# Performance work log

Measured on AMD Instinct MI355X. Metric: run time of the kernel, lower is better.

## Reference

```python
import jax, jax.numpy as jnp
import numpy as np

B, SEQ, PRED, DM = 16, 2048, 2048, 64
P = SEQ + PRED            # PointNum = 4096, per-node feature length
NLAYER, HID = 3, 4096     # MLPNums, ggdmodel hidden sizes
NH, HS = 16, 4096         # NumAttentionHeads, HiddenSize
G_CONST, K = 1.0, 8
NN = DM * DM              # 4096 == P, MHSA input dim (required by original code)


def setup_inputs() -> dict:
    key = jax.random.key(0)
    ks = jax.random.split(key, 11)
    s_mlp = 1.0 / np.sqrt(P).astype(np.float32)
    s_att = 1.0 / np.sqrt(NN).astype(np.float32)
    s_out = 1.0 / np.sqrt(HS).astype(np.float32)
    return {
        "x": jax.random.normal(ks[0], (B, P, DM), jnp.float32),
        "W_mlp": jax.random.normal(ks[1], (NLAYER, P, HID), jnp.float32) * s_mlp,
        "b_mlp": jnp.zeros((NLAYER, HID), jnp.float32),
        "Wq": jax.random.normal(ks[2], (NN, HS), jnp.float32) * s_att,
        "bq": jnp.zeros((HS,), jnp.float32),
        "Wk": jax.random.normal(ks[3], (NN, HS), jnp.float32) * s_att,
        "bk": jnp.zeros((HS,), jnp.float32),
        "Wv": jax.random.normal(ks[4], (NN, HS), jnp.float32) * s_att,
        "bv": jnp.zeros((HS,), jnp.float32),
        "Wo": jax.random.normal(ks[5], (HS, HS), jnp.float32) * s_out,
        "bo": jnp.zeros((HS,), jnp.float32),
    }


def _grav_adj(h):
    # h: [B, N, D] node features -> symmetrized, top-K masked gravity adjacency [B, N, N]
    norm = jnp.linalg.norm(h, axis=-1)                      # [B, N]
    m = jnp.sum(h, axis=-1) / norm                          # node "mass"
    sim = jnp.einsum('bnd,bmd->bnm', h, h) / (norm[:, :, None] * norm[:, None, :])
    F = G_CONST * m[:, :, None] * m[:, None, :] * sim * sim  # gravity matrix
    kth = jax.lax.top_k(F, K)[0][..., -1:]                  # per-row Kth largest value
    F = jnp.where(F >= kth, F, 0.0)                         # keep only top-K per row
    F = jnp.maximum(F, 0.0)                                 # ReLU
    return 0.5 * (F + jnp.swapaxes(F, -1, -2))              # symmetrize


def reference(x, W_mlp, b_mlp, Wq, bq, Wk, bk, Wv, bv, Wo, bo):
    h = jnp.swapaxes(x, 1, 2)                               # [B, N=DM, P]
    adjs = [_grav_adj(h)]
    for l in range(NLAYER):                                 # each MLP applied to the same h
        hv = h @ W_mlp[l] + b_mlp[l]                        # [B, N, HID]
        adjs.append(_grav_adj(hv))
    A = jnp.stack(adjs, axis=1)                             # [B, L, N, N], L = NLAYER + 1
    Lseq = A.shape[1]
    tok = A.reshape(B, Lseq, NN)                            # L tokens of dim N*N
    dh = HS // NH
    q = (tok @ Wq + bq).reshape(B, Lseq, NH, dh)
    k = (tok @ Wk + bk).reshape(B, Lseq, NH, dh)
    v = (tok @ Wv + bv).reshape(B, Lseq, NH, dh)
    scores = jnp.einsum('blhd,bmhd->bhlm', q, k) / np.sqrt(dh).astype(np.float32)
    attn = jax.nn.softmax(scores, axis=-1)
    ctx = jnp.einsum('bhlm,bmhd->blhd', attn, v).reshape(B, Lseq, HS)
    out = ctx @ Wo + bo                                     # [B, L, HS]
    return jnp.where(out > 0.5, out, 0.0)
```

## Files before the change

kernel.cpp:

```cpp
#include <hip/hip_runtime.h>
#include <math.h>


#define B16 16
#define PDIM 4096
#define NNODE 64
#define NCHUNK 32
#define KCG 128

typedef __attribute__((ext_vector_type(8))) short bf16x8;
typedef __attribute__((ext_vector_type(4))) float f32x4;
typedef __attribute__((ext_vector_type(4))) unsigned short us4;
typedef __attribute__((ext_vector_type(8))) unsigned short us8;

__device__ inline void split2(float x, unsigned short& h, unsigned short& l) {
  unsigned u = __float_as_uint(x);
  unsigned hu = (u + 0x7fffu + ((u >> 16) & 1u)) & 0xffff0000u;
  h = (unsigned short)(hu >> 16);
  float lo = x - __uint_as_float(hu);
  unsigned u2 = __float_as_uint(lo);
  l = (unsigned short)((u2 + 0x7fffu + ((u2 >> 16) & 1u)) >> 16);
}

__device__ inline void gload16(const void* g, void* lds) {
  __builtin_amdgcn_global_load_lds((const unsigned int*)g, (unsigned int*)lds, 16, 0, 0);
}

__global__ __launch_bounds__(256) void k_transpose(const float* __restrict__ x,
                                                   float* __restrict__ h,
                                                   unsigned short* __restrict__ AhT,
                                                   unsigned short* __restrict__ AlT,
                                                   int mode) {
  __shared__ float t[64][65];
  int b = blockIdx.y;
  int p0 = blockIdx.x * 64;
  const float* xb = x + (size_t)b * PDIM * NNODE;
#pragma unroll
  for (int i = 0; i < 16; ++i) {
    int e = i * 256 + threadIdx.x;
    int p = e >> 6, n = e & 63;
    t[p][n] = xb[(size_t)p0 * 64 + e];
  }
  __syncthreads();
  if (mode != 2) {
    float* hb = h + (size_t)b * NNODE * PDIM;
#pragma unroll
    for (int i = 0; i < 16; ++i) {
      int e = i * 256 + threadIdx.x;
      int n = e >> 6, p = e & 63;
      hb[(size_t)n * PDIM + p0 + p] = t[p][n];
    }
  }
  if (mode == 0) return;
#pragma unroll
  for (int j = 0; j < 2; ++j) {
    int cid = j * 256 + threadIdx.x;
    int n2 = cid >> 3, kg8 = cid & 7;
    us8 hv_, lv_;
#pragma unroll
    for (int e = 0; e < 8; ++e) {
      unsigned short hh, ll;
      split2(t[kg8 * 8 + e][n2], hh, ll);
      hv_[e] = hh; lv_[e] = ll;
    }
    int m = b * 64 + n2;
    int ks = (p0 >> 5) + (kg8 >> 2);
    size_t idx = (((size_t)(m >> 7) * 128 + ks) * 8 + ((m >> 4) & 7)) * 512 +
                 (size_t)((n2 & 15) + 16 * (kg8 & 3)) * 8;
    *(us8*)&AhT[idx] = hv_;
    *(us8*)&AlT[idx] = lv_;
  }
}

__global__ __launch_bounds__(256) void k_wsplit(const float* __restrict__ W,
                                                unsigned short* __restrict__ WhT,
                                                unsigned short* __restrict__ WlT) {
  __shared__ float Wt[32][132];
  int nb = blockIdx.x, kb = blockIdx.y;
  int tid = threadIdx.x;
#pragma unroll
  for (int i = 0; i < 4; ++i) {
    int idx = i * 256 + tid;
    int row = idx >> 5, c4 = idx & 31;
    float4 v = *(const float4*)&W[(size_t)(kb * 32 + row) * 4096 + nb * 128 + c4 * 4];
    *(float4*)&Wt[row][c4 * 4] = v;
  }
  __syncthreads();
#pragma unroll
  for (int j = 0; j < 2; ++j) {
    int cid = j * 256 + tid;
    int nl = cid & 127, kg = cid >> 7;
    us8 hv_, lv_;
#pragma unroll
    for (int e = 0; e < 8; ++e) {
      unsigned short hh, ll;
      split2(Wt[kg * 8 + e][nl], hh, ll);
      hv_[e] = hh; lv_[e] = ll;
    }
    size_t idx = (((size_t)nb * 128 + kb) * 8 + (nl >> 4)) * 512 +
                 (size_t)((nl & 15) + 16 * kg) * 8;
    *(us8*)&WhT[idx] = hv_;
    *(us8*)&WlT[idx] = lv_;
  }
}

__global__ __launch_bounds__(512, 4) void k_gemm_bf16(
    const unsigned short* __restrict__ Ah, const unsigned short* __restrict__ Al,
    const unsigned short* __restrict__ Bh, const unsigned short* __restrict__ Bl,
    float* __restrict__ Cp, int Ksteps, int ksplit, int N, int mstore) {
  __shared__ unsigned short sAh[2][4096], sAl[2][4096];
  __shared__ unsigned short sBh[2][4096], sBl[2][4096];
  int tid = threadIdx.x;
  int l = tid & 63, wid = tid >> 6;
  int wr = wid >> 2, wc = wid & 3;
  int nb = blockIdx.x, mb = blockIdx.y, z = blockIdx.z;
  int spp = Ksteps / ksplit;
  int ks0 = z * spp;

  const size_t abase = ((size_t)mb * Ksteps + ks0) * 4096 + tid * 8;
  const size_t bbase = ((size_t)nb * Ksteps + ks0) * 4096 + tid * 8;

  f32x4 acc[4][2];
#pragma unroll
  for (int i = 0; i < 4; ++i)
#pragma unroll
    for (int j = 0; j < 2; ++j) acc[i][j] = (f32x4){0.f, 0.f, 0.f, 0.f};

  gload16(Ah + abase, &sAh[0][tid * 8]);
  gload16(Al + abase, &sAl[0][tid * 8]);
  gload16(Bh + bbase, &sBh[0][tid * 8]);
  gload16(Bl + bbase, &sBl[0][tid * 8]);
  __syncthreads();

  int buf = 0;
  for (int t = 0; t < spp; ++t) {
    if (t + 1 < spp) {
      size_t off = (size_t)(t + 1) * 4096;
      gload16(Ah + abase + off, &sAh[buf ^ 1][tid * 8]);
      gload16(Al + abase + off, &sAl[buf ^ 1][tid * 8]);
      gload16(Bh + bbase + off, &sBh[buf ^ 1][tid * 8]);
      gload16(Bl + bbase + off, &sBl[buf ^ 1][tid * 8]);
    }
    bf16x8 ah[4], al4[4], bh2[2], bl2[2];
#pragma unroll
    for (int mt = 0; mt < 4; ++mt) {
      ah[mt]  = *(const bf16x8*)&sAh[buf][(wr * 4 + mt) * 512 + l * 8];
      al4[mt] = *(const bf16x8*)&sAl[buf][(wr * 4 + mt) * 512 + l * 8];
    }
#pragma unroll
    for (int nt = 0; nt < 2; ++nt) {
      bh2[nt] = *(const bf16x8*)&sBh[buf][(wc * 2 + nt) * 512 + l * 8];
      bl2[nt] = *(const bf16x8*)&sBl[buf][(wc * 2 + nt) * 512 + l * 8];
    }
#pragma unroll
    for (int mt = 0; mt < 4; ++mt)
#pragma unroll
      for (int nt = 0; nt < 2; ++nt) {
        acc[mt][nt] = __builtin_amdgcn_mfma_f32_16x16x32_bf16(ah[mt],  bh2[nt], acc[mt][nt], 0, 0, 0);
        acc[mt][nt] = __builtin_amdgcn_mfma_f32_16x16x32_bf16(ah[mt],  bl2[nt], acc[mt][nt], 0, 0, 0);
        acc[mt][nt] = __builtin_amdgcn_mfma_f32_16x16x32_bf16(al4[mt], bh2[nt], acc[mt][nt], 0, 0, 0);
      }
    __syncthreads();
    buf ^= 1;
  }

  int n0 = nb * 128, m0 = mb * 128;
  float* Cz = Cp + (size_t)z * mstore * N;
#pragma unroll
  for (int mt = 0; mt < 4; ++mt)
#pragma unroll
    for (int nt = 0; nt < 2; ++nt) {
      int col = n0 + wc * 32 + nt * 16 + (l & 15);
#pragma unroll
      for (int r = 0; r < 4; ++r) {
        int row = m0 + wr * 64 + mt * 16 + ((l >> 4) << 2) + r;
        if (row < mstore) Cz[(size_t)row * N + col] = acc[mt][nt][r];
      }
    }
}

__global__ __launch_bounds__(512) void k_gemm_wsf32(
    const unsigned short* __restrict__ Ah, const unsigned short* __restrict__ Al,
    const float* __restrict__ W0, const float* __restrict__ W1,
    const float* __restrict__ W2, float* __restrict__ Cp, int ksplit) {
  __shared__ unsigned short sAh[2][2048], sAl[2][2048];
  __shared__ unsigned short sBh[2][4096], sBl[2][4096];
  int tid = threadIdx.x;
  int l = tid & 63, wid = tid >> 6;
  int wr = wid >> 2, wc = wid & 3;
  int nb = blockIdx.x, z = blockIdx.z;
  int mat = z / ksplit, kz = z - mat * ksplit;
  const float* W = (mat == 0) ? W0 : ((mat == 1) ? W1 : W2);
  int nsteps = 128 / ksplit;
  int ks0 = kz * nsteps;
  int n0 = nb * 128;

  const float* wbase = W + (size_t)((l >> 4) * 8) * 4096 + n0 + wid * 16 + (l & 15);
  int sidx = wid * 512 + l * 8;

  f32x4 acc[2][2];
#pragma unroll
  for (int i = 0; i < 2; ++i)
#pragma unroll
    for (int j = 0; j < 2; ++j) acc[i][j] = (f32x4){0.f, 0.f, 0.f, 0.f};

  {
    if (tid < 256) gload16(Ah + (size_t)ks0 * 4096 + tid * 8, &sAh[0][tid * 8]);
    else           gload16(Al + (size_t)ks0 * 4096 + (tid - 256) * 8, &sAl[0][(tid - 256) * 8]);
    float wv[8];
#pragma unroll
    for (int e = 0; e < 8; ++e) wv[e] = wbase[(size_t)ks0 * 131072 + (size_t)e * 4096];
    us8 hi, lo;
#pragma unroll
    for (int e = 0; e < 8; ++e) {
      unsigned short hh, ll;
      split2(wv[e], hh, ll);
      hi[e] = hh; lo[e] = ll;
    }
    *(us8*)&sBh[0][sidx] = hi;
    *(us8*)&sBl[0][sidx] = lo;
  }
  __syncthreads();

  int buf = 0;
  for (int t = 0; t < nsteps; ++t) {
    bool more = (t + 1 < nsteps);
    float wv[8];
    if (more) {
      int ks = ks0 + t + 1;
      if (tid < 256) gload16(Ah + (size_t)ks * 4096 + tid * 8, &sAh[buf ^ 1][tid * 8]);
      else           gload16(Al + (size_t)ks * 4096 + (tid - 256) * 8, &sAl[buf ^ 1][(tid - 256) * 8]);
#pragma unroll
      for (int e = 0; e < 8; ++e) wv[e] = wbase[(size_t)ks * 131072 + (size_t)e * 4096];
    }
    bf16x8 aH[2], aL[2], bH[2], bL[2];
#pragma unroll
    for (int i = 0; i < 2; ++i) {
      aH[i] = *(const bf16x8*)&sAh[buf][(wr * 2 + i) * 512 + l * 8];
      aL[i] = *(const bf16x8*)&sAl[buf][(wr * 2 + i) * 512 + l * 8];
      bH[i] = *(const bf16x8*)&sBh[buf][(wc * 2 + i) * 512 + l * 8];
      bL[i] = *(const bf16x8*)&sBl[buf][(wc * 2 + i) * 512 + l * 8];
    }
#pragma unroll
    for (int i = 0; i < 2; ++i)
#pragma unroll
      for (int j = 0; j < 2; ++j) {
        acc[i][j] = __builtin_amdgcn_mfma_f32_16x16x32_bf16(aH[i], bH[j], acc[i][j], 0, 0, 0);
        acc[i][j] = __builtin_amdgcn_mfma_f32_16x16x32_bf16(aH[i], bL[j], acc[i][j], 0, 0, 0);
        acc[i][j] = __builtin_amdgcn_mfma_f32_16x16x32_bf16(aL[i], bH[j], acc[i][j], 0, 0, 0);
      }
    if (more) {
      us8 hi, lo;
#pragma unroll
      for (int e = 0; e < 8; ++e) {
        unsigned short hh, ll;
        split2(wv[e], hh, ll);
        hi[e] = hh; lo[e] = ll;
      }
      *(us8*)&sBh[buf ^ 1][sidx] = hi;
      *(us8*)&sBl[buf ^ 1][sidx] = lo;
    }
    __syncthreads();
    buf ^= 1;
  }

  float* Cz = Cp + (size_t)z * 262144;
#pragma unroll
  for (int i = 0; i < 2; ++i)
#pragma unroll
    for (int j = 0; j < 2; ++j) {
      int col = n0 + wc * 32 + j * 16 + (l & 15);
#pragma unroll
      for (int r = 0; r < 4; ++r) {
        int row = (wr * 2 + i) * 16 + ((l >> 4) << 2) + r;
        Cz[(size_t)row * 4096 + col] = acc[i][j][r];
      }
    }
}

__global__ __launch_bounds__(256) void k_red_mlp_split(const float* __restrict__ Cp,
                                                       const float* __restrict__ bias,
                                                       unsigned short* __restrict__ hvh,
                                                       unsigned short* __restrict__ hvl) {
  int c = blockIdx.x * 256 + threadIdx.x;
  int m = c >> 9, kc = c & 511;
  int k0 = kc * 8;
  const float* p = Cp + (size_t)m * 4096 + k0;
  us8 hv_, lv_;
#pragma unroll
  for (int e = 0; e < 8; ++e) {
    float v = p[e] + p[e + 4194304] + bias[k0 + e];
    unsigned short hh, ll;
    split2(v, hh, ll);
    hv_[e] = hh; lv_[e] = ll;
  }
  int batch = m >> 6, rr = m & 63;
  size_t idx = (size_t)batch * 262144 + (size_t)(kc >> 2) * 2048 +
               (size_t)(rr >> 4) * 512 + (size_t)((rr & 15) + 16 * (kc & 3)) * 8;
  *(us8*)&hvh[idx] = hv_;
  *(us8*)&hvl[idx] = lv_;
}

__global__ __launch_bounds__(256) void k_gram_mfma(
    const unsigned short* __restrict__ Zh, const unsigned short* __restrict__ Zl,
    float* __restrict__ Gp, float* __restrict__ Sp,
    int bs1, int ks_stride, int nsteps) {
  __shared__ unsigned short sZh[2][2048], sZl[2][2048];
  int z = blockIdx.x, b = blockIdx.y;
  int tid = threadIdx.x;
  int l = tid & 63, w = tid >> 6;
  size_t zbase = (size_t)(b >> 1) * 524288 + (size_t)(b & 1) * bs1;
  int ks0 = z * nsteps;

  f32x4 acc[4], racc;
#pragma unroll
  for (int j = 0; j < 4; ++j) acc[j] = (f32x4){0.f, 0.f, 0.f, 0.f};
  racc = (f32x4){0.f, 0.f, 0.f, 0.f};
  bf16x8 ones;
#pragma unroll
  for (int e = 0; e < 8; ++e) ones[e] = (short)0x3F80;

  gload16(Zh + zbase + (size_t)ks0 * ks_stride + tid * 8, &sZh[0][tid * 8]);
  gload16(Zl + zbase + (size_t)ks0 * ks_stride + tid * 8, &sZl[0][tid * 8]);
  __syncthreads();

  int buf = 0;
  for (int t = 0; t < nsteps; ++t) {
    if (t + 1 < nsteps) {
      size_t off = zbase + (size_t)(ks0 + t + 1) * ks_stride + tid * 8;
      gload16(Zh + off, &sZh[buf ^ 1][tid * 8]);
      gload16(Zl + off, &sZl[buf ^ 1][tid * 8]);
    }
    bf16x8 bh[4], bl4[4];
#pragma unroll
    for (int nt = 0; nt < 4; ++nt) {
      bh[nt]  = *(const bf16x8*)&sZh[buf][nt * 512 + l * 8];
      bl4[nt] = *(const bf16x8*)&sZl[buf][nt * 512 + l * 8];
    }
    bf16x8 ah = bh[w], al = bl4[w];
#pragma unroll
    for (int nt = 0; nt < 4; ++nt) {
      acc[nt] = __builtin_amdgcn_mfma_f32_16x16x32_bf16(ah, bh[nt], acc[nt], 0, 0, 0);
      acc[nt] = __builtin_amdgcn_mfma_f32_16x16x32_bf16(ah, bl4[nt], acc[nt], 0, 0, 0);
      acc[nt] = __builtin_amdgcn_mfma_f32_16x16x32_bf16(al, bh[nt], acc[nt], 0, 0, 0);
    }
    racc = __builtin_amdgcn_mfma_f32_16x16x32_bf16(ah, ones, racc, 0, 0, 0);
    racc = __builtin_amdgcn_mfma_f32_16x16x32_bf16(al, ones, racc, 0, 0, 0);
    __syncthreads();
    buf ^= 1;
  }

  float* Gz = Gp + ((size_t)z * B16 + b) * 4096;
#pragma unroll
  for (int nt = 0; nt < 4; ++nt) {
    int col = nt * 16 + (l & 15);
#pragma unroll
    for (int r = 0; r < 4; ++r) {
      int row = w * 16 + ((l >> 4) << 2) + r;
      Gz[row * 64 + col] = acc[nt][r];
    }
  }
  if ((l & 15) == 0) {
    float* Sz = Sp + ((size_t)z * B16 + b) * 64;
#pragma unroll
    for (int r = 0; r < 4; ++r) Sz[w * 16 + ((l >> 4) << 2) + r] = racc[r];
  }
}

__global__ __launch_bounds__(256) void k_gred8(const float* __restrict__ Gp,
                                               const float* __restrict__ Sp,
                                               float* __restrict__ G,
                                               float* __restrict__ S, int slot) {
  int idx = blockIdx.x * 256 + threadIdx.x;
  if (idx < 65536) {
    float s = 0.f;
#pragma unroll
    for (int c = 0; c < 8; ++c) s += Gp[(size_t)c * 65536 + idx];
    G[(size_t)slot * 65536 + idx] = s;
  } else if (idx < 66560) {
    int i2 = idx - 65536;
    float s = 0.f;
#pragma unroll
    for (int c = 0; c < 8; ++c) s += Sp[(size_t)c * 1024 + i2];
    S[(size_t)slot * 1024 + i2] = s;
  }
}

__global__ __launch_bounds__(256) void k_redN(const float* __restrict__ Cp,
                                              const float* __restrict__ bias,
                                              float* __restrict__ dst,
                                              int nparts, int thr) {
  int idx = blockIdx.x * 256 + threadIdx.x;
  float s = bias[idx & 4095];
  for (int p = 0; p < nparts; ++p) s += Cp[(size_t)p * 262144 + idx];
  if (thr) s = (s > 0.5f) ? s : 0.f;
  dst[idx] = s;
}

__device__ inline float wmax64(float v) {
#pragma unroll
  for (int off = 32; off; off >>= 1) v = fmaxf(v, __shfl_xor(v, off));
  return v;
}

__global__ __launch_bounds__(256) void k_adj_t(const float* __restrict__ G,
                                               const float* __restrict__ S,
                                               unsigned short* __restrict__ tokh,
                                               unsigned short* __restrict__ tokl) {
  __shared__ float Fm[64][64];
  __shared__ float nrm[64], mm[64];
  int b = blockIdx.x >> 2, lz = blockIdx.x & 3;
  int tid = threadIdx.x;
  int j = tid & 63, w = tid >> 6;
  const float* Gb = G + ((size_t)lz * B16 + b) * 4096;
  const float* Sb = S + ((size_t)lz * B16 + b) * 64;
  if (tid < 64) {
    float nj = sqrtf(Gb[tid * 64 + tid]);
    nrm[tid] = nj;
    mm[tid] = Sb[tid] / nj;
  }
  __syncthreads();
  for (int i = w; i < 64; i += 4) {
    float g = Gb[i * 64 + j];
    float sim = g / (nrm[i] * nrm[j]);
    Fm[i][j] = mm[i] * mm[j] * sim * sim;
  }
  __syncthreads();
  for (int i = w; i < 64; i += 4) {
    float f = Fm[i][j];
    int cnt = 0;
#pragma unroll
    for (int u4 = 0; u4 < 16; ++u4) {
      float4 q = *(const float4*)&Fm[i][u4 * 4];
      cnt += (q.x > f) + (q.y > f) + (q.z > f) + (q.w > f);
    }
    float cand = (cnt <= 7) ? f : INFINITY;
#pragma unroll
    for (int off = 32; off; off >>= 1) cand = fminf(cand, __shfl_xor(cand, off));
    float fm = (f >= cand) ? fmaxf(f, 0.f) : 0.f;
    Fm[i][j] = fm;
  }
  __syncthreads();
  int r = b * 4 + lz;
  int mt = r >> 4, rl = r & 15;
#pragma unroll
  for (int c = 0; c < 2; ++c) {
    int cid = tid * 2 + c;
    int jj0 = cid >> 3, g = cid & 7;
    us8 hv_, lv_;
#pragma unroll
    for (int e = 0; e < 8; ++e) {
      int kcol = g * 8 + e;
      float val = 0.5f * (Fm[jj0][kcol] + Fm[kcol][jj0]);
      unsigned short hh, ll;
      split2(val, hh, ll);
      hv_[e] = hh; lv_[e] = ll;
    }
    int ks = jj0 * 2 + (g >> 2);
    size_t idx = ((size_t)ks * 8 + mt) * 512 + (size_t)(rl + 16 * (g & 3)) * 8;
    *(us8*)&tokh[idx] = hv_;
    *(us8*)&tokl[idx] = lv_;
  }
}

__global__ __launch_bounds__(64) void k_attn_t(const float* __restrict__ q,
                                               const float* __restrict__ k,
                                               const float* __restrict__ v,
                                               unsigned short* __restrict__ ctxh,
                                               unsigned short* __restrict__ ctxl) {
  __shared__ float cb[4][256];
  int hd = blockIdx.x, b = blockIdx.y;
  int t = threadIdx.x;
  float qr[4][4], kr[4][4], vr[4][4];
#pragma unroll
  for (int l = 0; l < 4; ++l)
#pragma unroll
    for (int s = 0; s < 4; ++s) {
      size_t off = ((size_t)(b * 4 + l)) * 4096 + hd * 256 + t + s * 64;
      qr[l][s] = q[off]; kr[l][s] = k[off]; vr[l][s] = v[off];
    }
  float sc[4][4];
#pragma unroll
  for (int l = 0; l < 4; ++l)
#pragma unroll
    for (int m = 0; m < 4; ++m) {
      float p = 0.f;
#pragma unroll
      for (int s = 0; s < 4; ++s) p = fmaf(qr[l][s], kr[m][s], p);
#pragma unroll
      for (int off = 32; off; off >>= 1) p += __shfl_xor(p, off);
      sc[l][m] = p * (1.0f / 16.0f);
    }
  float at[4][4];
#pragma unroll
  for (int l = 0; l < 4; ++l) {
    float mx = fmaxf(fmaxf(sc[l][0], sc[l][1]), fmaxf(sc[l][2], sc[l][3]));
    float e0 = expf(sc[l][0] - mx), e1 = expf(sc[l][1] - mx);
    float e2 = expf(sc[l][2] - mx), e3 = expf(sc[l][3] - mx);
    float d = e0 + e1 + e2 + e3;
    at[l][0] = e0 / d; at[l][1] = e1 / d; at[l][2] = e2 / d; at[l][3] = e3 / d;
  }
#pragma unroll
  for (int l = 0; l < 4; ++l)
#pragma unroll
    for (int s = 0; s < 4; ++s) {
      float c = 0.f;
#pragma unroll
      for (int m = 0; m < 4; ++m) c = fmaf(at[l][m], vr[m][s], c);
      cb[l][s * 64 + t] = c;
    }
  __syncthreads();
  int lq = t >> 4, c16 = t & 15;
  int mt = b >> 2, rl = (b & 3) * 4 + lq;
#pragma unroll
  for (int e8 = 0; e8 < 2; ++e8) {
    us8 hv_, lv_;
#pragma unroll
    for (int e = 0; e < 8; ++e) {
      unsigned short hh, ll;
      split2(cb[lq][c16 * 16 + e8 * 8 + e], hh, ll);
      hv_[e] = hh; lv_[e] = ll;
    }
    int ks = hd * 8 + (c16 >> 1);
    size_t idx = ((size_t)ks * 8 + mt) * 512 + (size_t)(rl + 16 * ((c16 * 2 + e8) & 3)) * 8;
    *(us8*)&ctxh[idx] = hv_;
    *(us8*)&ctxl[idx] = lv_;
  }
}

__global__ __launch_bounds__(256) void k_gram_partial(const float* __restrict__ Z,
                                                      float* __restrict__ Gp,
                                                      float* __restrict__ Sp) {
  __shared__ float Zt[KCG][68];
  int c = blockIdx.x, b = blockIdx.y;
  int tid = threadIdx.x;
  const float* Zb = Z + (size_t)b * NNODE * PDIM + c * KCG;
#pragma unroll
  for (int i = 0; i < 32; ++i) {
    int e = i * 256 + tid;
    int r = e >> 7, kk = e & 127;
    Zt[kk][r] = Zb[(size_t)r * PDIM + kk];
  }
  __syncthreads();
  int ii = tid >> 2, j0 = (tid & 3) << 4;
  float acc[16] = {};
  for (int kk = 0; kk < KCG; ++kk) {
    float zi = Zt[kk][ii];
    float4 z0 = *(const float4*)&Zt[kk][j0 + 0];
    float4 z1 = *(const float4*)&Zt[kk][j0 + 4];
    float4 z2 = *(const float4*)&Zt[kk][j0 + 8];
    float4 z3 = *(const float4*)&Zt[kk][j0 + 12];
    acc[0] = fmaf(zi, z0.x, acc[0]);   acc[1] = fmaf(zi, z0.y, acc[1]);
    acc[2] = fmaf(zi, z0.z, acc[2]);   acc[3] = fmaf(zi, z0.w, acc[3]);
    acc[4] = fmaf(zi, z1.x, acc[4]);   acc[5] = fmaf(zi, z1.y, acc[5]);
    acc[6] = fmaf(zi, z1.z, acc[6]);   acc[7] = fmaf(zi, z1.w, acc[7]);
    acc[8] = fmaf(zi, z2.x, acc[8]);   acc[9] = fmaf(zi, z2.y, acc[9]);
    acc[10] = fmaf(zi, z2.z, acc[10]); acc[11] = fmaf(zi, z2.w, acc[11]);
    acc[12] = fmaf(zi, z3.x, acc[12]); acc[13] = fmaf(zi, z3.y, acc[13]);
    acc[14] = fmaf(zi, z3.z, acc[14]); acc[15] = fmaf(zi, z3.w, acc[15]);
  }
  float* gp = Gp + ((size_t)c * B16 + b) * 4096 + ii * 64 + j0;
#pragma unroll
  for (int j = 0; j < 16; ++j) gp[j] = acc[j];
  if (tid < 64) {
    float s = 0.f;
    for (int kk = 0; kk < KCG; ++kk) s += Zt[kk][tid];
    Sp[((size_t)c * B16 + b) * 64 + tid] = s;
  }
}

__global__ __launch_bounds__(256) void k_gram_reduce(const float* __restrict__ Gp,
                                                     const float* __restrict__ Sp,
                                                     float* __restrict__ G,
                                                     float* __restrict__ S, int slot) {
  int idx = blockIdx.x * 256 + threadIdx.x;
  if (idx < B16 * 4096) {
    float s = 0.f;
    for (int c = 0; c < NCHUNK; ++c) s += Gp[(size_t)c * (B16 * 4096) + idx];
    G[(size_t)slot * (B16 * 4096) + idx] = s;
  } else {
    int idx2 = idx - B16 * 4096;
    float s = 0.f;
    for (int c = 0; c < NCHUNK; ++c) s += Sp[(size_t)c * (B16 * 64) + idx2];
    S[(size_t)slot * (B16 * 64) + idx2] = s;
  }
}

__global__ __launch_bounds__(256) void k_gemm_mfma(
    const float* __restrict__ A, const float* __restrict__ B0,
    const float* __restrict__ B1, const float* __restrict__ B2,
    const float* __restrict__ bias, float* __restrict__ C,
    int mrows, int mstore, int N, int K, int ksplit) {
  __shared__ __align__(16) unsigned short sA[2][8][64][8];
  __shared__ __align__(16) unsigned short sB[2][8][64][8];
  int z = blockIdx.z;
  int mat = z / ksplit, ks = z - mat * ksplit;
  const float* Bm = (mat == 0) ? B0 : ((mat == 1) ? B1 : B2);
  int kchunk = K / ksplit;
  int k0 = ks * kchunk, k1 = k0 + kchunk;
  int tid = threadIdx.x;
  int l = tid & 63;
  int wr = (tid >> 7) & 1, wc = (tid >> 6) & 1;
  int m0 = blockIdx.y * 128, n0g = blockIdx.x * 128;
  bool activeM = (m0 + wr * 64) < mstore;
  int am = tid >> 1;
  int arow = m0 + am; if (arow >= mrows) arow = mrows - 1;
  const float* Arow = A + (size_t)arow * K;
  int amt = am >> 4;
  int bk = tid >> 3;
  int bnb = (tid & 7) * 4;
  int bg = bk >> 3, bslot = bk & 7;
  f32x4 acc[4][4];
#pragma unroll
  for (int i = 0; i < 4; ++i)
#pragma unroll
    for (int j = 0; j < 4; ++j) acc[i][j] = (f32x4){0.f, 0.f, 0.f, 0.f};
  for (int kb = k0; kb < k1; kb += 32) {
    __syncthreads();
#pragma unroll
    for (int i = 0; i < 4; ++i) {
      int kq = (tid & 1) * 4 + i * 8;
      float4 a = *(const float4*)(Arow + kb + kq);
      unsigned short h0, h1, h2, h3, l0, l1, l2, l3;
      split2(a.x, h0, l0); split2(a.y, h1, l1);
      split2(a.z, h2, l2); split2(a.w, h3, l3);
      int lane_t = (am & 15) + 16 * (kq >> 3);
      int sb = kq & 4;
      *(us4*)&sA[0][amt][lane_t][sb] = (us4){h0, h1, h2, h3};
      *(us4*)&sA[1][amt][lane_t][sb] = (us4){l0, l1, l2, l3};
    }
    {
      const float* Brow = Bm + (size_t)(kb + bk) * N + n0g;
#pragma unroll
      for (int i = 0; i < 4; ++i) {
        int n = bnb + i * 32;
        int nt = n >> 4, nr = n & 15;
        float4 b = *(const float4*)(Brow + n);
        float be[4] = {b.x, b.y, b.z, b.w};
#pragma unroll
        for (int e = 0; e < 4; ++e) {
          unsigned short hh, ll;
          split2(be[e], hh, ll);
          sB[0][nt][nr + e + 16 * bg][bslot] = hh;
          sB[1][nt][nr + e + 16 * bg][bslot] = ll;
        }
      }
    }
    __syncthreads();
    if (!activeM) continue;
    bf16x8 ah[4], al[4], bh[4], bl[4];
#pragma unroll
    for (int t = 0; t < 4; ++t) {
      ah[t] = *(const bf16x8*)&sA[0][wr * 4 + t][l][0];
      al[t] = *(const bf16x8*)&sA[1][wr * 4 + t][l][0];
      bh[t] = *(const bf16x8*)&sB[0][wc * 4 + t][l][0];
      bl[t] = *(const bf16x8*)&sB[1][wc * 4 + t][l][0];
    }
#pragma unroll
    for (int mt = 0; mt < 4; ++mt)
#pragma unroll
      for (int nt = 0; nt < 4; ++nt) {
        acc[mt][nt] = __builtin_amdgcn_mfma_f32_16x16x32_bf16(ah[mt], bh[nt], acc[mt][nt], 0, 0, 0);
        acc[mt][nt] = __builtin_amdgcn_mfma_f32_16x16x32_bf16(ah[mt], bl[nt], acc[mt][nt], 0, 0, 0);
        acc[mt][nt] = __builtin_amdgcn_mfma_f32_16x16x32_bf16(al[mt], bh[nt], acc[mt][nt], 0, 0, 0);
      }
  }
  if (!activeM) return;
  float* Cz = C + (size_t)z * mstore * N;
#pragma unroll
  for (int mt = 0; mt < 4; ++mt)
#pragma unroll
    for (int nt = 0; nt < 4; ++nt) {
      int col = n0g + wc * 64 + nt * 16 + (l & 15);
      float badd = bias ? bias[col] : 0.f;
#pragma unroll
      for (int r = 0; r < 4; ++r) {
        int row = m0 + wr * 64 + mt * 16 + ((l >> 4) << 2) + r;
        if (row < mstore) Cz[(size_t)row * N + col] = acc[mt][nt][r] + badd;
      }
    }
}

__global__ __launch_bounds__(64) void k_adj_fb(const float* __restrict__ G,
                                               const float* __restrict__ S,
                                               float* __restrict__ tok) {
  __shared__ float Fm[64][64];
  __shared__ float nrm[64], mm[64];
  int b = blockIdx.x >> 2, lz = blockIdx.x & 3;
  int j = threadIdx.x;
  const float* Gb = G + ((size_t)lz * B16 + b) * 4096;
  const float* Sb = S + ((size_t)lz * B16 + b) * 64;
  float nj = sqrtf(Gb[j * 64 + j]);
  nrm[j] = nj;
  mm[j] = Sb[j] / nj;
  __syncthreads();
  for (int i = 0; i < 64; ++i) {
    float g = Gb[i * 64 + j];
    float sim = g / (nrm[i] * nj);
    float F = mm[i] * mm[j] * sim * sim;
    float v = F;
    bool act = true;
    float kth = 0.f;
#pragma unroll
    for (int it = 0; it < 8; ++it) {
      float mv = wmax64(act ? v : -INFINITY);
      kth = mv;
      unsigned long long ball = __ballot(act && (v == mv));
      int first = __ffsll(ball) - 1;
      if (j == first) act = false;
    }
    float fm = (F >= kth) ? F : 0.f;
    Fm[i][j] = fmaxf(fm, 0.f);
  }
  __syncthreads();
  float* tb = tok + ((size_t)b * 4 + lz) * 4096;
  for (int i = 0; i < 64; ++i) tb[i * 64 + j] = 0.5f * (Fm[i][j] + Fm[j][i]);
}

__global__ __launch_bounds__(256) void k_qkv_reduce(const float* __restrict__ Cp,
                                                    const float* __restrict__ bq,
                                                    const float* __restrict__ bk,
                                                    const float* __restrict__ bv,
                                                    float* __restrict__ q,
                                                    float* __restrict__ k,
                                                    float* __restrict__ v) {
  int idx = blockIdx.x * 256 + threadIdx.x;
  int mat = idx >> 18;
  int rn = idx & ((1 << 18) - 1);
  int n = rn & 4095;
  const float* base = Cp + (size_t)mat * 4 * 262144;
  float s = base[rn] + base[rn + 262144] + base[rn + 2 * 262144] + base[rn + 3 * 262144];
  if (mat == 0) q[rn] = s + bq[n];
  else if (mat == 1) k[rn] = s + bk[n];
  else v[rn] = s + bv[n];
}

__global__ __launch_bounds__(64) void k_attn_fb(const float* __restrict__ q,
                                                const float* __restrict__ k,
                                                const float* __restrict__ v,
                                                float* __restrict__ ctx) {
  int hd = blockIdx.x, b = blockIdx.y;
  int t = threadIdx.x;
  float qr[4][4], kr[4][4], vr[4][4];
#pragma unroll
  for (int l = 0; l < 4; ++l)
#pragma unroll
    for (int s = 0; s < 4; ++s) {
      size_t off = ((size_t)(b * 4 + l)) * 4096 + hd * 256 + t + s * 64;
      qr[l][s] = q[off]; kr[l][s] = k[off]; vr[l][s] = v[off];
    }
  float sc[4][4];
#pragma unroll
  for (int l = 0; l < 4; ++l)
#pragma unroll
    for (int m = 0; m < 4; ++m) {
      float p = 0.f;
#pragma unroll
      for (int s = 0; s < 4; ++s) p = fmaf(qr[l][s], kr[m][s], p);
#pragma unroll
      for (int off = 32; off; off >>= 1) p += __shfl_xor(p, off);
      sc[l][m] = p * (1.0f / 16.0f);
    }
  float at[4][4];
#pragma unroll
  for (int l = 0; l < 4; ++l) {
    float mx = fmaxf(fmaxf(sc[l][0], sc[l][1]), fmaxf(sc[l][2], sc[l][3]));
    float e0 = expf(sc[l][0] - mx), e1 = expf(sc[l][1] - mx);
    float e2 = expf(sc[l][2] - mx), e3 = expf(sc[l][3] - mx);
    float d = e0 + e1 + e2 + e3;
    at[l][0] = e0 / d; at[l][1] = e1 / d; at[l][2] = e2 / d; at[l][3] = e3 / d;
  }
#pragma unroll
  for (int l = 0; l < 4; ++l)
#pragma unroll
    for (int s = 0; s < 4; ++s) {
      float c = 0.f;
#pragma unroll
      for (int m = 0; m < 4; ++m) c = fmaf(at[l][m], vr[m][s], c);
      ctx[((size_t)(b * 4 + l)) * 4096 + hd * 256 + t + s * 64] = c;
    }
}

__global__ __launch_bounds__(256) void k_out_reduce(const float* __restrict__ Cp,
                                                    const float* __restrict__ bo,
                                                    float* __restrict__ out) {
  int idx = blockIdx.x * 256 + threadIdx.x;
  int n = idx & 4095;
  float s = bo[n];
#pragma unroll
  for (int p = 0; p < 8; ++p) s += Cp[(size_t)p * 262144 + idx];
  out[idx] = (s > 0.5f) ? s : 0.f;
}

extern "C" void kernel_launch(void* const* d_in, const int* in_sizes, int n_in,
                              void* d_out, int out_size, void* d_ws, size_t ws_size,
                              hipStream_t stream) {
  const float* x     = (const float*)d_in[0];
  const float* W_mlp = (const float*)d_in[1];
  const float* b_mlp = (const float*)d_in[2];
  const float* Wq = (const float*)d_in[3]; const float* bq = (const float*)d_in[4];
  const float* Wk = (const float*)d_in[5]; const float* bk = (const float*)d_in[6];
  const float* Wv = (const float*)d_in[7]; const float* bv = (const float*)d_in[8];
  const float* Wo = (const float*)d_in[9]; const float* bo = (const float*)d_in[10];
  float* out = (float*)d_out;
  float* ws = (float*)d_ws;

  float* h   = ws;
  float* Gp  = ws + 8388608;
  float* Sp  = ws + 10485760;
  float* G   = ws + 10518528;
  float* S   = ws + 10780672;

  const size_t NEED = 41979904ull * 4ull;
  if (ws_size >= NEED) {
    unsigned short* hvh = (unsigned short*)(ws + 4194304);
    unsigned short* hvl = (unsigned short*)(ws + 6291456);
    float* q   = ws + 10784768;
    float* kk  = ws + 11046912;
    float* vv  = ws + 11309056;
    unsigned short* AhT = (unsigned short*)(ws + 11571200);
    unsigned short* AlT = (unsigned short*)(ws + 13668352);
    unsigned short* WhT = (unsigned short*)(ws + 15765504);
    unsigned short* WlT = (unsigned short*)(ws + 24154112);
    float* Cp           = ws + 32542720;
    unsigned short* tokh = (unsigned short*)(ws + 40931328);
    unsigned short* tokl = (unsigned short*)(ws + 41193472);
    unsigned short* ctxh = (unsigned short*)(ws + 41455616);
    unsigned short* ctxl = (unsigned short*)(ws + 41717760);

    k_transpose<<<dim3(64, 16), 256, 0, stream>>>(x, h, AhT, AlT, 2);

    k_gram_mfma<<<dim3(8, 16), 256, 0, stream>>>(AhT, AlT, Gp, Sp, 2048, 4096, 16);
    k_gred8<<<260, 256, 0, stream>>>(Gp, Sp, G, S, 0);

    for (int l = 0; l < 3; ++l) {
      k_wsplit<<<dim3(32, 128), 256, 0, stream>>>(W_mlp + (size_t)l * 16777216, WhT, WlT);
      k_gemm_bf16<<<dim3(32, 8, 2), 512, 0, stream>>>(AhT, AlT, WhT, WlT, Cp,
                                                      128, 2, 4096, 1024);
      k_red_mlp_split<<<2048, 256, 0, stream>>>(Cp, b_mlp + (size_t)l * 4096, hvh, hvl);
      k_gram_mfma<<<dim3(8, 16), 256, 0, stream>>>(hvh, hvl, Gp, Sp, 262144, 2048, 16);
      k_gred8<<<260, 256, 0, stream>>>(Gp, Sp, G, S, l + 1);
    }

    k_adj_t<<<64, 256, 0, stream>>>(G, S, tokh, tokl);

    k_gemm_wsf32<<<dim3(32, 1, 24), 512, 0, stream>>>(tokh, tokl, Wq, Wk, Wv, Cp, 8);
    k_redN<<<1024, 256, 0, stream>>>(Cp,                bq, q,  8, 0);
    k_redN<<<1024, 256, 0, stream>>>(Cp + 8 * 262144,   bk, kk, 8, 0);
    k_redN<<<1024, 256, 0, stream>>>(Cp + 16 * 262144,  bv, vv, 8, 0);

    k_attn_t<<<dim3(16, 16), 64, 0, stream>>>(q, kk, vv, ctxh, ctxl);

    k_gemm_wsf32<<<dim3(32, 1, 8), 512, 0, stream>>>(ctxh, ctxl, Wo, Wo, Wo, Cp, 8);
    k_redN<<<1024, 256, 0, stream>>>(Cp, bo, out, 8, 1);
  } else {
    float* hv  = ws + 4194304;
    float* tok = ws + 10784768;
    float* q   = ws + 11046912;
    float* kk  = ws + 11309056;
    float* vv  = ws + 11571200;
    float* ctx = ws + 11833344;
    float* qkvp = hv;
    float* op   = h;

    k_transpose<<<dim3(64, 16), 256, 0, stream>>>(x, h, (unsigned short*)0,
                                                  (unsigned short*)0, 0);
    k_gram_partial<<<dim3(NCHUNK, 16), 256, 0, stream>>>(h, Gp, Sp);
    k_gram_reduce<<<260, 256, 0, stream>>>(Gp, Sp, G, S, 0);
    for (int l = 0; l < 3; ++l) {
      const float* Wl = W_mlp + (size_t)l * PDIM * 4096;
      const float* bl = b_mlp + (size_t)l * 4096;
      k_gemm_mfma<<<dim3(32, 8, 1), 256, 0, stream>>>(h, Wl, Wl, Wl, bl, hv,
                                                      1024, 1024, 4096, 4096, 1);
      k_gram_partial<<<dim3(NCHUNK, 16), 256, 0, stream>>>(hv, Gp, Sp);
      k_gram_reduce<<<260, 256, 0, stream>>>(Gp, Sp, G, S, l + 1);
    }
    k_adj_fb<<<64, 64, 0, stream>>>(G, S, tok);
    k_gemm_mfma<<<dim3(32, 1, 12), 256, 0, stream>>>(tok, Wq, Wk, Wv, nullptr, qkvp,
                                                     64, 64, 4096, 4096, 4);
    k_qkv_reduce<<<3072, 256, 0, stream>>>(qkvp, bq, bk, bv, q, kk, vv);
    k_attn_fb<<<dim3(16, 16), 64, 0, stream>>>(q, kk, vv, ctx);
    k_gemm_mfma<<<dim3(32, 1, 8), 256, 0, stream>>>(ctx, Wo, Wo, Wo, nullptr, op,
                                                    64, 64, 4096, 4096, 8);
    k_out_reduce<<<1024, 256, 0, stream>>>(op, bo, out);
  }
}
```

Before: 642.6 us.

## Enlarge MLP GEMM tile to 256x256 with 1024 threads and fuse QKV reductions

The MLP GEMM now uses 256x256 output tiles per block with 16 waves, each wave computing a 64x64 sub-tile, and raises the K-split from 2 to 4. The larger tile increases operand reuse from LDS and halves the global loads per output element. The bigger split-K keeps enough blocks in flight, at the cost of a larger partial buffer and a 4-way reduction. The three q/k/v bias reductions are also merged into one launch to cut launch overhead. The change needs a larger workspace and uses 128KB of LDS per block, which limits occupancy to one block per CU.

```diff
diff --git a/kernel.cpp b/kernel.cpp
--- a/kernel.cpp
+++ b/kernel.cpp
@@ -104,78 +104,75 @@
   }
 }
 
-__global__ __launch_bounds__(512, 4) void k_gemm_bf16(
+__global__ __launch_bounds__(1024) void k_gemm_mlp(
     const unsigned short* __restrict__ Ah, const unsigned short* __restrict__ Al,
     const unsigned short* __restrict__ Bh, const unsigned short* __restrict__ Bl,
-    float* __restrict__ Cp, int Ksteps, int ksplit, int N, int mstore) {
-  __shared__ unsigned short sAh[2][4096], sAl[2][4096];
-  __shared__ unsigned short sBh[2][4096], sBl[2][4096];
+    float* __restrict__ Cp) {
+  __shared__ unsigned short sAh[2][8192], sAl[2][8192];
+  __shared__ unsigned short sBh[2][8192], sBl[2][8192];
   int tid = threadIdx.x;
   int l = tid & 63, wid = tid >> 6;
   int wr = wid >> 2, wc = wid & 3;
   int nb = blockIdx.x, mb = blockIdx.y, z = blockIdx.z;
-  int spp = Ksteps / ksplit;
+  const int spp = 32;
   int ks0 = z * spp;
 
-  const size_t abase = ((size_t)mb * Ksteps + ks0) * 4096 + tid * 8;
-  const size_t bbase = ((size_t)nb * Ksteps + ks0) * 4096 + tid * 8;
-
-  f32x4 acc[4][2];
+  int half = tid >> 9, off8 = (tid & 511) * 8;
+  size_t gA = (size_t)(mb * 2 + half) * 128;
+  size_t gB = (size_t)(nb * 2 + half) * 128;
+
+  f32x4 acc[4][4];
 #pragma unroll
   for (int i = 0; i < 4; ++i)
 #pragma unroll
-    for (int j = 0; j < 2; ++j) acc[i][j] = (f32x4){0.f, 0.f, 0.f, 0.f};
-
-  gload16(Ah + abase, &sAh[0][tid * 8]);
-  gload16(Al + abase, &sAl[0][tid * 8]);
-  gload16(Bh + bbase, &sBh[0][tid * 8]);
-  gload16(Bl + bbase, &sBl[0][tid * 8]);
+    for (int j = 0; j < 4; ++j) acc[i][j] = (f32x4){0.f, 0.f, 0.f, 0.f};
+
+  gload16(Ah + (gA + ks0) * 4096 + off8, &sAh[0][tid * 8]);
+  gload16(Al + (gA + ks0) * 4096 + off8, &sAl[0][tid * 8]);
+  gload16(Bh + (gB + ks0) * 4096 + off8, &sBh[0][tid * 8]);
+  gload16(Bl + (gB + ks0) * 4096 + off8, &sBl[0][tid * 8]);
   __syncthreads();
 
   int buf = 0;
   for (int t = 0; t < spp; ++t) {
     if (t + 1 < spp) {
-      size_t off = (size_t)(t + 1) * 4096;
-      gload16(Ah + abase + off, &sAh[buf ^ 1][tid * 8]);
-      gload16(Al + abase + off, &sAl[buf ^ 1][tid * 8]);
-      gload16(Bh + bbase + off, &sBh[buf ^ 1][tid * 8]);
-      gload16(Bl + bbase + off, &sBl[buf ^ 1][tid * 8]);
-    }
-    bf16x8 ah[4], al4[4], bh2[2], bl2[2];
-#pragma unroll
-    for (int mt = 0; mt < 4; ++mt) {
-      ah[mt]  = *(const bf16x8*)&sAh[buf][(wr * 4 + mt) * 512 + l * 8];
-      al4[mt] = *(const bf16x8*)&sAl[buf][(wr * 4 + mt) * 512 + l * 8];
-    }
-#pragma unroll
-    for (int nt = 0; nt < 2; ++nt) {
-      bh2[nt] = *(const bf16x8*)&sBh[buf][(wc * 2 + nt) * 512 + l * 8];
-      bl2[nt] = *(const bf16x8*)&sBl[buf][(wc * 2 + nt) * 512 + l * 8];
+      size_t ks = ks0 + t + 1;
+      gload16(Ah + (gA + ks) * 4096 + off8, &sAh[buf ^ 1][tid * 8]);
+      gload16(Al + (gA + ks) * 4096 + off8, &sAl[buf ^ 1][tid * 8]);
+      gload16(Bh + (gB + ks) * 4096 + off8, &sBh[buf ^ 1][tid * 8]);
+      gload16(Bl + (gB + ks) * 4096 + off8, &sBl[buf ^ 1][tid * 8]);
+    }
+    bf16x8 ah[4], al4[4], bh4[4], bl4[4];
+#pragma unroll
+    for (int i = 0; i < 4; ++i) {
+      ah[i]  = *(const bf16x8*)&sAh[buf][(wr * 4 + i) * 512 + l * 8];
+      al4[i] = *(const bf16x8*)&sAl[buf][(wr * 4 + i) * 512 + l * 8];
+      bh4[i] = *(const bf16x8*)&sBh[buf][(wc * 4 + i) * 512 + l * 8];
+      bl4[i] = *(const bf16x8*)&sBl[buf][(wc * 4 + i) * 512 + l * 8];
     }
 #pragma unroll
     for (int mt = 0; mt < 4; ++mt)
 #pragma unroll
-      for (int nt = 0; nt < 2; ++nt) {
-        acc[mt][nt] = __builtin_amdgcn_mfma_f32_16x16x32_bf16(ah[mt],  bh2[nt], acc[mt][nt], 0, 0, 0);
-        acc[mt][nt] = __builtin_amdgcn_mfma_f32_16x16x32_bf16(ah[mt],  bl2[nt], acc[mt][nt], 0, 0, 0);
-        acc[mt][nt] = __builtin_amdgcn_mfma_f32_16x16x32_bf16(al4[mt], bh2[nt], acc[mt][nt], 0, 0, 0);
+      for (int nt = 0; nt < 4; ++nt) {
+        acc[mt][nt] = __builtin_amdgcn_mfma_f32_16x16x32_bf16(ah[mt],  bh4[nt], acc[mt][nt], 0, 0, 0);
+        acc[mt][nt] = __builtin_amdgcn_mfma_f32_16x16x32_bf16(ah[mt],  bl4[nt], acc[mt][nt], 0, 0, 0);
+        acc[mt][nt] = __builtin_amdgcn_mfma_f32_16x16x32_bf16(al4[mt], bh4[nt], acc[mt][nt], 0, 0, 0);
       }
     __syncthreads();
     buf ^= 1;
   }
 
-  int n0 = nb * 128, m0 = mb * 128;
-  float* Cz = Cp + (size_t)z * mstore * N;
+  int n0 = nb * 256, m0 = mb * 256;
+  float* Cz = Cp + (size_t)z * (1024 * 4096);
 #pragma unroll
   for (int mt = 0; mt < 4; ++mt)
 #pragma unroll
-    for (int nt = 0; nt < 2; ++nt) {
-      int col = n0 + wc * 32 + nt * 16 + (l & 15);
-#pragma unroll
-      for (int r = 0; r < 4; ++r) {
-        int row = m0 + wr * 64 + mt * 16 + ((l >> 4) << 2) + r;
-        if (row < mstore) Cz[(size_t)row * N + col] = acc[mt][nt][r];
-      }
+    for (int nt = 0; nt < 4; ++nt) {
+      int col = n0 + wc * 64 + nt * 16 + (l & 15);
+      int rowb = m0 + wr * 64 + mt * 16 + ((l >> 4) << 2);
+#pragma unroll
+      for (int r = 0; r < 4; ++r)
+        Cz[(size_t)(rowb + r) * 4096 + col] = acc[mt][nt][r];
     }
 }
 
@@ -289,7 +286,7 @@
   us8 hv_, lv_;
 #pragma unroll
   for (int e = 0; e < 8; ++e) {
-    float v = p[e] + p[e + 4194304] + bias[k0 + e];
+    float v = p[e] + p[e + 4194304] + p[e + 2 * 4194304] + p[e + 3 * 4194304] + bias[k0 + e];
     unsigned short hh, ll;
     split2(v, hh, ll);
     hv_[e] = hh; lv_[e] = ll;
@@ -384,6 +381,26 @@
     for (int c = 0; c < 8; ++c) s += Sp[(size_t)c * 1024 + i2];
     S[(size_t)slot * 1024 + i2] = s;
   }
+}
+
+__global__ __launch_bounds__(256) void k_redqkv8(const float* __restrict__ Cp,
+                                                 const float* __restrict__ bq,
+                                                 const float* __restrict__ bk,
+                                                 const float* __restrict__ bv,
+                                                 float* __restrict__ q,
+                                                 float* __restrict__ k,
+                                                 float* __restrict__ v) {
+  int idx = blockIdx.x * 256 + threadIdx.x;
+  int mat = idx >> 18;
+  int rn = idx & ((1 << 18) - 1);
+  int n = rn & 4095;
+  const float* base = Cp + (size_t)mat * 8 * 262144;
+  float s = 0.f;
+#pragma unroll
+  for (int p = 0; p < 8; ++p) s += base[(size_t)p * 262144 + rn];
+  if (mat == 0) q[rn] = s + bq[n];
+  else if (mat == 1) k[rn] = s + bk[n];
+  else v[rn] = s + bv[n];
 }
 
 __global__ __launch_bounds__(256) void k_redN(const float* __restrict__ Cp,
@@ -811,7 +828,7 @@
   float* G   = ws + 10518528;
   float* S   = ws + 10780672;
 
-  const size_t NEED = 41979904ull * 4ull;
+  const size_t NEED = 50368512ull * 4ull;
   if (ws_size >= NEED) {
     unsigned short* hvh = (unsigned short*)(ws + 4194304);
     unsigned short* hvl = (unsigned short*)(ws + 6291456);
@@ -823,10 +840,10 @@
     unsigned short* WhT = (unsigned short*)(ws + 15765504);
     unsigned short* WlT = (unsigned short*)(ws + 24154112);
     float* Cp           = ws + 32542720;
-    unsigned short* tokh = (unsigned short*)(ws + 40931328);
-    unsigned short* tokl = (unsigned short*)(ws + 41193472);
-    unsigned short* ctxh = (unsigned short*)(ws + 41455616);
-    unsigned short* ctxl = (unsigned short*)(ws + 41717760);
+    unsigned short* tokh = (unsigned short*)(ws + 49319936);
+    unsigned short* tokl = (unsigned short*)(ws + 49582080);
+    unsigned short* ctxh = (unsigned short*)(ws + 49844224);
+    unsigned short* ctxl = (unsigned short*)(ws + 50106368);
 
     k_transpose<<<dim3(64, 16), 256, 0, stream>>>(x, h, AhT, AlT, 2);
 
@@ -835,8 +852,7 @@
 
     for (int l = 0; l < 3; ++l) {
       k_wsplit<<<dim3(32, 128), 256, 0, stream>>>(W_mlp + (size_t)l * 16777216, WhT, WlT);
-      k_gemm_bf16<<<dim3(32, 8, 2), 512, 0, stream>>>(AhT, AlT, WhT, WlT, Cp,
-                                                      128, 2, 4096, 1024);
+      k_gemm_mlp<<<dim3(16, 4, 4), 1024, 0, stream>>>(AhT, AlT, WhT, WlT, Cp);
       k_red_mlp_split<<<2048, 256, 0, stream>>>(Cp, b_mlp + (size_t)l * 4096, hvh, hvl);
       k_gram_mfma<<<dim3(8, 16), 256, 0, stream>>>(hvh, hvl, Gp, Sp, 262144, 2048, 16);
       k_gred8<<<260, 256, 0, stream>>>(Gp, Sp, G, S, l + 1);
@@ -845,9 +861,7 @@
     k_adj_t<<<64, 256, 0, stream>>>(G, S, tokh, tokl);
 
     k_gemm_wsf32<<<dim3(32, 1, 24), 512, 0, stream>>>(tokh, tokl, Wq, Wk, Wv, Cp, 8);
-    k_redN<<<1024, 256, 0, stream>>>(Cp,                bq, q,  8, 0);
-    k_redN<<<1024, 256, 0, stream>>>(Cp + 8 * 262144,   bk, kk, 8, 0);
-    k_redN<<<1024, 256, 0, stream>>>(Cp + 16 * 262144,  bv, vv, 8, 0);
+    k_redqkv8<<<3072, 256, 0, stream>>>(Cp, bq, bk, bv, q, kk, vv);
 
     k_attn_t<<<dim3(16, 16), 64, 0, stream>>>(q, kk, vv, ctxh, ctxl);
 
```

Result: no change. 654.8 us (+1.9%).
